# Kernel tuning notes

Hardware: AMD Instinct MI355X
Metric: run time of the kernel (lower is better)

The kernel has to match this reference:

```python
import jax, jax.numpy as jnp
import numpy as np

DIM = 1024
HEADS = 16
DIM_HEAD = 64
NB_FEATURES = 266
EPS = 1e-4


def _gaussian_orthogonal_random_matrix(nb_rows, nb_cols, seed=0):
    # Blocks of orthogonal rows (QR of gaussian), rows rescaled by gaussian row norms (scaling=0).
    rng = np.random.default_rng(seed)
    blocks = []
    full, rem = divmod(nb_rows, nb_cols)
    for _ in range(full):
        g = rng.standard_normal((nb_cols, nb_cols))
        q, _ = np.linalg.qr(g)
        blocks.append(q.T)
    if rem > 0:
        g = rng.standard_normal((nb_cols, nb_cols))
        q, _ = np.linalg.qr(g)
        blocks.append(q.T[:rem])
    mat = np.concatenate(blocks, axis=0)
    multiplier = np.linalg.norm(rng.standard_normal((nb_rows, nb_cols)), axis=1)
    return (multiplier[:, None] * mat).astype(np.float32)


def _softmax_kernel(data, proj, is_query):
    # data: [b,h,n,d], proj: [m,d]
    d = data.shape[-1]
    data_normalizer = d ** -0.25
    ratio = proj.shape[0] ** -0.5
    data_dash = jnp.einsum('bhnd,md->bhnm', data * data_normalizer, proj)
    diag = 0.5 * (data_normalizer ** 2) * jnp.sum(data * data, axis=-1, keepdims=True)
    if is_query:
        m = jax.lax.stop_gradient(jnp.max(data_dash, axis=-1, keepdims=True))
    else:
        m = jax.lax.stop_gradient(jnp.max(data_dash, axis=(-1, -2), keepdims=True))
    return ratio * (jnp.exp(data_dash - diag - m) + EPS)


def _linear_attention(q, k, v):
    # q,k: [b,h,n,m], v: [b,h,n,e]
    k_cumsum = jnp.sum(k, axis=-2)                                   # [b,h,m]
    D_inv = 1.0 / jnp.einsum('bhnm,bhm->bhn', q, k_cumsum)           # [b,h,n]
    context = jnp.einsum('bhnm,bhne->bhme', k, v)                    # [b,h,m,e]
    return jnp.einsum('bhme,bhnm,bhn->bhne', context, q, D_inv)      # [b,h,n,e]


def setup_inputs() -> dict:
    key = jax.random.key(0)
    k1, k2, k3, k4, k5 = jax.random.split(key, 5)
    B, N = 2, 4096
    inner = HEADS * DIM_HEAD
    s = DIM ** -0.5
    return {
        'x': jax.random.normal(k1, (B, N, DIM), dtype=jnp.float32),
        'Wq': jax.random.normal(k2, (inner, DIM), dtype=jnp.float32) * s,
        'Wk': jax.random.normal(k3, (inner, DIM), dtype=jnp.float32) * s,
        'Wv': jax.random.normal(k4, (inner, DIM), dtype=jnp.float32) * s,
        'Wo': jax.random.normal(k5, (DIM, inner), dtype=jnp.float32) * s,
        'bo': jnp.zeros((DIM,), dtype=jnp.float32),
        'proj': jnp.asarray(_gaussian_orthogonal_random_matrix(NB_FEATURES, DIM_HEAD)),
    }


def reference(x, Wq, Wk, Wv, Wo, bo, proj):
    b, n, _ = x.shape
    def split_heads(t):
        return t.reshape(b, n, HEADS, DIM_HEAD).transpose(0, 2, 1, 3)  # [b,h,n,d]
    q = split_heads(x @ Wq.T)
    k = split_heads(x @ Wk.T)
    v = split_heads(x @ Wv.T)
    qp = _softmax_kernel(q, proj, is_query=True)
    kp = _softmax_kernel(k, proj, is_query=False)
    out = _linear_attention(qp, kp, v)                                # [b,h,n,d]
    out = out.transpose(0, 2, 1, 3).reshape(b, n, HEADS * DIM_HEAD)
    return out @ Wo.T + bo
```

## Files before the change

### kernel.cpp

```cpp
#include <hip/hip_runtime.h>
#include <hip/hip_bf16.h>
#include <hip/hip_fp16.h>


#define B_   2
#define N_   4096
#define H_   16
#define M_   266
#define MP_  288
#define DIM_ 1024
#define RT_  8192
#define BH_  32
#define LKN  40
#define LSB  296
#define NCH  16
#define KS_  8

typedef __attribute__((ext_vector_type(8))) short s8v;
typedef __attribute__((ext_vector_type(4))) float f4v;

__device__ __forceinline__ ushort f2bu(float x){ __hip_bfloat16 h = __float2bfloat16(x); return *(ushort*)&h; }
__device__ __forceinline__ float  bu2f(ushort u){ return __uint_as_float(((unsigned)u) << 16); }

constexpr float NORMC  = 0.35355339059327379f;
constexpr float RATIOC = 0.06131393f;
constexpr float DIAGC  = 0.0625f;
constexpr float EPSC   = 1e-4f;

__device__ __forceinline__ void stf(float* p, float v){ *p = v; }
__device__ __forceinline__ void stf(__hip_bfloat16* p, float v){ *p = __float2bfloat16(v); }

__device__ __forceinline__ void gl_lds16(const ushort* g, ushort* l){
    __builtin_amdgcn_global_load_lds(
        (const __attribute__((address_space(1))) unsigned int*)(const unsigned int*)g,
        (__attribute__((address_space(3))) unsigned int*)(unsigned int*)l,
        16, 0, 0);
}

__device__ __forceinline__ void cast8(const float* __restrict__ s, ushort* __restrict__ d, int i){
    const float4 a = *(const float4*)&s[i];
    const float4 b = *(const float4*)&s[i + 4];
    ushort4 lo, hi;
    lo.x = f2bu(a.x); lo.y = f2bu(a.y); lo.z = f2bu(a.z); lo.w = f2bu(a.w);
    hi.x = f2bu(b.x); hi.y = f2bu(b.y); hi.z = f2bu(b.z); hi.w = f2bu(b.w);
    *(ushort4*)&d[i]     = lo;
    *(ushort4*)&d[i + 4] = hi;
}

__global__ void cast_all(const float* __restrict__ x,
                         const float* __restrict__ Wq, const float* __restrict__ Wk,
                         const float* __restrict__ Wv, const float* __restrict__ Wo,
                         const float* __restrict__ proj,
                         ushort* __restrict__ xb,
                         ushort* __restrict__ Wqb, ushort* __restrict__ Wkb,
                         ushort* __restrict__ Wvb, ushort* __restrict__ Wob,
                         ushort* __restrict__ projb)
{
    const int bid = blockIdx.x, tid = threadIdx.x;
    if (bid < 4096) {
        cast8(x, xb, (bid * 256 + tid) * 8);
    } else if (bid < 6144) {
        const int w = (bid - 4096) >> 9;
        const float* s; ushort* d;
        switch (w) {
            case 0:  s = Wq; d = Wqb; break;
            case 1:  s = Wk; d = Wkb; break;
            case 2:  s = Wv; d = Wvb; break;
            default: s = Wo; d = Wob; break;
        }
        cast8(s, d, (((bid - 4096) & 511) * 256 + tid) * 8);
    } else {
        const int i = (bid - 6144) * 256 + tid;
        const int m = i >> 6, dc = i & 63;
        projb[i] = f2bu((m < M_) ? NORMC * proj[m * 64 + dc] : 0.f);
    }
}

template<bool DIAG, bool BIAS, typename TC>
__launch_bounds__(256)
__global__ void gemm128(const ushort* __restrict__ A, const ushort* __restrict__ Bw,
                        const float* __restrict__ bias, TC* __restrict__ C,
                        float* __restrict__ diag)
{
    __shared__ ushort As[128 * 32];
    __shared__ ushort Bs[128 * 32];

    const int tid  = threadIdx.x;
    const int lane = tid & 63, wave = tid >> 6;
    const int col  = lane & 15, quad = lane >> 4;
    const int wm   = (wave & 1) * 64, wn = (wave >> 1) * 64;

    const int gX = gridDim.x, total = gX * gridDim.y, cpx = total >> 3;
    const int fl = blockIdx.x + blockIdx.y * gX;
    const int sw = (fl & 7) * cpx + (fl >> 3);
    const int r0 = (sw / gX) * 128, c0 = (sw % gX) * 128;

    const int f0 = tid * 8;
    const int row0 = f0 >> 5, kc0 = f0 & 31;
    const size_t aoff0 = (size_t)(r0 + row0) * DIM_ + kc0;
    const size_t aoff1 = (size_t)(r0 + 64 + row0) * DIM_ + kc0;
    const size_t boff0 = (size_t)(c0 + row0) * DIM_ + kc0;
    const size_t boff1 = (size_t)(c0 + 64 + row0) * DIM_ + kc0;
    ushort* asb0 = &As[wave * 512];
    ushort* asb1 = &As[2048 + wave * 512];
    ushort* bsb0 = &Bs[wave * 512];
    ushort* bsb1 = &Bs[2048 + wave * 512];

    f4v acc[4][4];
    #pragma unroll
    for (int i = 0; i < 4; ++i)
        #pragma unroll
        for (int j = 0; j < 4; ++j) acc[i][j] = (f4v){0.f, 0.f, 0.f, 0.f};

    for (int kk = 0; kk < DIM_; kk += 32) {
        gl_lds16(&A[aoff0 + kk],  asb0);
        gl_lds16(&A[aoff1 + kk],  asb1);
        gl_lds16(&Bw[boff0 + kk], bsb0);
        gl_lds16(&Bw[boff1 + kk], bsb1);
        __syncthreads();
        s8v af[4], bf[4];
        #pragma unroll
        for (int i = 0; i < 4; ++i)
            af[i] = *(const s8v*)&As[(wm + i * 16 + col) * 32 + quad * 8];
        #pragma unroll
        for (int j = 0; j < 4; ++j)
            bf[j] = *(const s8v*)&Bs[(wn + j * 16 + col) * 32 + quad * 8];
        #pragma unroll
        for (int i = 0; i < 4; ++i)
            #pragma unroll
            for (int j = 0; j < 4; ++j)
                acc[i][j] = __builtin_amdgcn_mfma_f32_16x16x32_bf16(af[i], bf[j], acc[i][j], 0, 0, 0);
        __syncthreads();
    }

    float bb[4] = {0.f, 0.f, 0.f, 0.f};
    if (BIAS) {
        #pragma unroll
        for (int j = 0; j < 4; ++j) bb[j] = bias[c0 + wn + j * 16 + col];
    }
    #pragma unroll
    for (int i = 0; i < 4; ++i) {
        #pragma unroll
        for (int r = 0; r < 4; ++r) {
            const size_t grow = (size_t)(r0 + wm + i * 16 + quad * 4 + r);
            #pragma unroll
            for (int j = 0; j < 4; ++j)
                stf(&C[grow * DIM_ + c0 + wn + j * 16 + col], acc[i][j][r] + bb[j]);
        }
    }
    if (DIAG) {
        const int hglob = (c0 + wn) >> 6;
        #pragma unroll
        for (int i = 0; i < 4; ++i) {
            #pragma unroll
            for (int r = 0; r < 4; ++r) {
                float s = 0.f;
                #pragma unroll
                for (int j = 0; j < 4; ++j) s += acc[i][j][r] * acc[i][j][r];
                s += __shfl_xor(s, 1); s += __shfl_xor(s, 2);
                s += __shfl_xor(s, 4); s += __shfl_xor(s, 8);
                if (col == 0)
                    diag[(size_t)(r0 + wm + i * 16 + quad * 4 + r) * H_ + hglob] = DIAGC * s;
            }
        }
    }
}

__launch_bounds__(256)
__global__ void gemm128_qkv(const ushort* __restrict__ A, const ushort* __restrict__ Bw,
                            ushort* __restrict__ Q, ushort* __restrict__ K,
                            ushort* __restrict__ V,
                            float* __restrict__ diagQ, float* __restrict__ diagK)
{
    __shared__ ushort As[128 * 32];
    __shared__ ushort Bs[128 * 32];

    const int tid  = threadIdx.x;
    const int lane = tid & 63, wave = tid >> 6;
    const int col  = lane & 15, quad = lane >> 4;
    const int wm   = (wave & 1) * 64, wn = (wave >> 1) * 64;

    const int fl = blockIdx.x + blockIdx.y * 24;
    const int sw = (fl & 7) * 192 + (fl >> 3);
    const int r0 = (sw / 24) * 128, c0 = (sw % 24) * 128;

    const int f0 = tid * 8;
    const int row0 = f0 >> 5, kc0 = f0 & 31;
    const size_t aoff0 = (size_t)(r0 + row0) * DIM_ + kc0;
    const size_t aoff1 = (size_t)(r0 + 64 + row0) * DIM_ + kc0;
    const size_t boff0 = (size_t)(c0 + row0) * DIM_ + kc0;
    const size_t boff1 = (size_t)(c0 + 64 + row0) * DIM_ + kc0;
    ushort* asb0 = &As[wave * 512];
    ushort* asb1 = &As[2048 + wave * 512];
    ushort* bsb0 = &Bs[wave * 512];
    ushort* bsb1 = &Bs[2048 + wave * 512];

    f4v acc[4][4];
    #pragma unroll
    for (int i = 0; i < 4; ++i)
        #pragma unroll
        for (int j = 0; j < 4; ++j) acc[i][j] = (f4v){0.f, 0.f, 0.f, 0.f};

    for (int kk = 0; kk < DIM_; kk += 32) {
        gl_lds16(&A[aoff0 + kk],  asb0);
        gl_lds16(&A[aoff1 + kk],  asb1);
        gl_lds16(&Bw[boff0 + kk], bsb0);
        gl_lds16(&Bw[boff1 + kk], bsb1);
        __syncthreads();
        s8v af[4], bf[4];
        #pragma unroll
        for (int i = 0; i < 4; ++i)
            af[i] = *(const s8v*)&As[(wm + i * 16 + col) * 32 + quad * 8];
        #pragma unroll
        for (int j = 0; j < 4; ++j)
            bf[j] = *(const s8v*)&Bs[(wn + j * 16 + col) * 32 + quad * 8];
        #pragma unroll
        for (int i = 0; i < 4; ++i)
            #pragma unroll
            for (int j = 0; j < 4; ++j)
                acc[i][j] = __builtin_amdgcn_mfma_f32_16x16x32_bf16(af[i], bf[j], acc[i][j], 0, 0, 0);
        __syncthreads();
    }

    const int which = c0 >> 10;
    const int cc    = c0 & 1023;
    ushort* C = (which == 0) ? Q : ((which == 1) ? K : V);
    float* dptr = (which == 0) ? diagQ : ((which == 1) ? diagK : nullptr);

    #pragma unroll
    for (int i = 0; i < 4; ++i) {
        #pragma unroll
        for (int r = 0; r < 4; ++r) {
            const size_t grow = (size_t)(r0 + wm + i * 16 + quad * 4 + r);
            #pragma unroll
            for (int j = 0; j < 4; ++j)
                C[grow * DIM_ + cc + wn + j * 16 + col] = f2bu(acc[i][j][r]);
        }
    }
    if (dptr) {
        const int hglob = (cc + wn) >> 6;
        #pragma unroll
        for (int i = 0; i < 4; ++i) {
            #pragma unroll
            for (int r = 0; r < 4; ++r) {
                float s = 0.f;
                #pragma unroll
                for (int j = 0; j < 4; ++j) s += acc[i][j][r] * acc[i][j][r];
                s += __shfl_xor(s, 1); s += __shfl_xor(s, 2);
                s += __shfl_xor(s, 4); s += __shfl_xor(s, 8);
                if (col == 0)
                    dptr[(size_t)(r0 + wm + i * 16 + quad * 4 + r) * H_ + hglob] = DIAGC * s;
            }
        }
    }
}

__launch_bounds__(256)
__global__ void kctx_mfma(const ushort* __restrict__ Kb, const ushort* __restrict__ Vb,
                          const ushort* __restrict__ projb,
                          const float* __restrict__ diagK,
                          float* __restrict__ ctxp, float* __restrict__ kcsp,
                          float* __restrict__ vsump, float* __restrict__ kmaxp)
{
    __shared__ ushort Pl[MP_ * 64];
    __shared__ ushort Kp[MP_ * LKN];
    __shared__ ushort Vt[64 * LKN];
    __shared__ float kred[2][MP_];
    __shared__ float wmx[4];

    const int tid  = threadIdx.x;
    const int lane = tid & 63, wave = tid >> 6;
    const int col  = lane & 15, quad = lane >> 4;
    const int bh   = blockIdx.y, b = bh >> 4, h = bh & 15;
    const int n0   = blockIdx.x * (N_ / NCH);
    const int rowblk = wave >> 1;
    const int t0 = (wave & 1) * 9;

    for (int i = tid; i < MP_ * 8; i += 256) {
        const int m = i >> 3, c = i & 7;
        *(uint4*)&Pl[m * 64 + ((c ^ (m & 7)) << 3)] = *(const uint4*)&projb[m * 64 + (c << 3)];
    }
    const int sw0 = (quad ^ (col & 7)) << 3;
    const int sw1 = ((quad | 4) ^ (col & 7)) << 3;
    __syncthreads();

    float mx = -3.4e38f;
    {
        size_t arA = ((size_t)(b * N_ + n0 + rowblk * 16 + col)) * DIM_ + h * 64 + quad * 8;
        s8v pA0 = *(const s8v*)&Kb[arA];
        s8v pA1 = *(const s8v*)&Kb[arA + 32];
        for (int ks = 0; ks < KS_; ++ks) {
            const s8v a0 = pA0, a1 = pA1;
            if (ks + 1 < KS_) {
                arA += (size_t)32 * DIM_;
                pA0 = *(const s8v*)&Kb[arA];
                pA1 = *(const s8v*)&Kb[arA + 32];
            }
            for (int t = t0; t < t0 + 9; ++t) {
                const s8v bf0 = *(const s8v*)&Pl[(t * 16 + col) * 64 + sw0];
                const s8v bf1 = *(const s8v*)&Pl[(t * 16 + col) * 64 + sw1];
                f4v a = (f4v){0.f, 0.f, 0.f, 0.f};
                a = __builtin_amdgcn_mfma_f32_16x16x32_bf16(a0, bf0, a, 0, 0, 0);
                a = __builtin_amdgcn_mfma_f32_16x16x32_bf16(a1, bf1, a, 0, 0, 0);
                if (t * 16 + col < M_) {
                    #pragma unroll
                    for (int r = 0; r < 4; ++r) mx = fmaxf(mx, a[r]);
                }
            }
        }
    }
    #pragma unroll
    for (int o = 32; o > 0; o >>= 1) mx = fmaxf(mx, __shfl_xor(mx, o));
    if (lane == 0) wmx[wave] = mx;
    __syncthreads();
    const float mc = fmaxf(fmaxf(wmx[0], wmx[1]), fmaxf(wmx[2], wmx[3]));
    if (tid == 0) kmaxp[bh * NCH + blockIdx.x] = mc;

    const int nst = tid & 31, est = (tid >> 5) * 8;
    s8v vvP = *(const s8v*)&Vb[((size_t)(b * N_ + n0 + nst)) * DIM_ + h * 64 + est];
    const size_t arow0 = ((size_t)(b * N_ + n0 + rowblk * 16 + col)) * DIM_ + h * 64 + quad * 8;
    s8v afP0 = *(const s8v*)&Kb[arow0];
    s8v afP1 = *(const s8v*)&Kb[arow0 + 32];
    float dgrP[4];
    #pragma unroll
    for (int r = 0; r < 4; ++r)
        dgrP[r] = diagK[((size_t)(b * N_ + n0 + rowblk * 16 + quad * 4 + r)) * H_ + h];

    f4v facc[18];
    #pragma unroll
    for (int t = 0; t < 18; ++t) facc[t] = (f4v){0.f, 0.f, 0.f, 0.f};
    float kcsa[9] = {};
    float vsa[8] = {};

    for (int ks = 0; ks < KS_; ++ks) {
        const s8v vv = vvP, af0 = afP0, af1 = afP1;
        float dgr[4];
        #pragma unroll
        for (int r = 0; r < 4; ++r) dgr[r] = dgrP[r];

        #pragma unroll
        for (int j = 0; j < 8; ++j) {
            const ushort uv = ((const ushort*)&vv)[j];
            Vt[(est + j) * LKN + nst] = uv;
            vsa[j] += bu2f(uv);
        }

        for (int t = t0; t < t0 + 9; ++t) {
            const s8v bf0 = *(const s8v*)&Pl[(t * 16 + col) * 64 + sw0];
            const s8v bf1 = *(const s8v*)&Pl[(t * 16 + col) * 64 + sw1];
            f4v a = (f4v){0.f, 0.f, 0.f, 0.f};
            a = __builtin_amdgcn_mfma_f32_16x16x32_bf16(af0, bf0, a, 0, 0, 0);
            a = __builtin_amdgcn_mfma_f32_16x16x32_bf16(af1, bf1, a, 0, 0, 0);
            const int m = t * 16 + col;
            float kp[4];
            #pragma unroll
            for (int r = 0; r < 4; ++r) {
                float v = 0.f;
                if (m < M_) v = __expf(a[r] - dgr[r] - mc);
                kp[r] = v;
            }
            kcsa[t - t0] += kp[0] + kp[1] + kp[2] + kp[3];
            ushort4 pk;
            pk.x = f2bu(kp[0]); pk.y = f2bu(kp[1]); pk.z = f2bu(kp[2]); pk.w = f2bu(kp[3]);
            *(ushort4*)&Kp[m * LKN + rowblk * 16 + quad * 4] = pk;
        }

        if (ks + 1 < KS_) {
            const int nb1 = n0 + (ks + 1) * 32;
            vvP  = *(const s8v*)&Vb[((size_t)(b * N_ + nb1 + nst)) * DIM_ + h * 64 + est];
            const size_t arow1 = ((size_t)(b * N_ + nb1 + rowblk * 16 + col)) * DIM_ + h * 64 + quad * 8;
            afP0 = *(const s8v*)&Kb[arow1];
            afP1 = *(const s8v*)&Kb[arow1 + 32];
            #pragma unroll
            for (int r = 0; r < 4; ++r)
                dgrP[r] = diagK[((size_t)(b * N_ + nb1 + rowblk * 16 + quad * 4 + r)) * H_ + h];
        }
        __syncthreads();
        const s8v bfe = *(const s8v*)&Vt[(wave * 16 + col) * LKN + quad * 8];
        #pragma unroll
        for (int t = 0; t < 18; ++t) {
            const s8v am = *(const s8v*)&Kp[(t * 16 + col) * LKN + quad * 8];
            facc[t] = __builtin_amdgcn_mfma_f32_16x16x32_bf16(am, bfe, facc[t], 0, 0, 0);
        }
        __syncthreads();
    }

    const size_t pbase = ((size_t)bh * NCH + blockIdx.x) * (MP_ * 64);
    #pragma unroll
    for (int t = 0; t < 18; ++t) {
        #pragma unroll
        for (int r = 0; r < 4; ++r)
            __builtin_nontemporal_store(facc[t][r],
                &ctxp[pbase + (size_t)(t * 16 + quad * 4 + r) * 64 + wave * 16 + col]);
    }
    #pragma unroll
    for (int j = 0; j < 8; ++j) {
        float s = vsa[j];
        s += __shfl_xor(s, 1);  s += __shfl_xor(s, 2);
        s += __shfl_xor(s, 4);  s += __shfl_xor(s, 8);
        s += __shfl_xor(s, 16);
        if ((lane & 31) == 0)
            vsump[((size_t)bh * NCH + blockIdx.x) * 64 + est + j] = s;
    }
    for (int t = t0; t < t0 + 9; ++t) {
        float s = kcsa[t - t0];
        s += __shfl_xor(s, 16);
        s += __shfl_xor(s, 32);
        if (quad == 0) kred[rowblk][t * 16 + col] = s;
    }
    __syncthreads();
    for (int i = tid; i < MP_; i += 256)
        kcsp[((size_t)bh * NCH + blockIdx.x) * MP_ + i] = kred[0][i] + kred[1][i];
}

__launch_bounds__(256)
__global__ void ctx_reduce(const float* __restrict__ ctxp, const float* __restrict__ kcsp,
                           const float* __restrict__ vsump, const float* __restrict__ kmaxp,
                           ushort* __restrict__ ctxT, float* __restrict__ kcs)
{
    __shared__ float scl[NCH];
    __shared__ float vsl[64];
    const int bh = blockIdx.y, tid = threadIdx.x;

    if (tid < NCH) {
        float M = -3.4e38f;
        #pragma unroll
        for (int c = 0; c < NCH; ++c) M = fmaxf(M, kmaxp[bh * NCH + c]);
        scl[tid] = __expf(kmaxp[bh * NCH + tid] - M);
    }
    if (tid >= 64 && tid < 128) {
        const int e = tid - 64;
        float s = 0.f;
        #pragma unroll
        for (int c = 0; c < NCH; ++c) s += vsump[((size_t)bh * NCH + c) * 64 + e];
        vsl[e] = s;
    }
    __syncthreads();

    const int base = blockIdx.x * (MP_ * 64 / 8);
    const size_t cb = (size_t)bh * NCH * (MP_ * 64);
    #pragma unroll
    for (int u = 0; u < 9; ++u) {
        const int flat = base + u * 256 + tid;
        float s = 0.f;
        #pragma unroll
        for (int c = 0; c < NCH; ++c)
            s += scl[c] * __builtin_nontemporal_load(&ctxp[cb + (size_t)c * (MP_ * 64) + flat]);
        const int m = flat >> 6, e = flat & 63;
        ctxT[((size_t)bh * 64 + e) * MP_ + m] = f2bu(RATIOC * (s + EPSC * vsl[e]));
    }
    if (blockIdx.x == 0) {
        for (int i = tid; i < MP_; i += 256) {
            float s = 0.f;
            #pragma unroll
            for (int c = 0; c < NCH; ++c) s += scl[c] * kcsp[((size_t)bh * NCH + c) * MP_ + i];
            kcs[(size_t)bh * MP_ + i] = RATIOC * (s + EPSC * (float)N_);
        }
    }
}

__launch_bounds__(256)
__global__ void qdashout(const ushort* __restrict__ Qb, const ushort* __restrict__ projb,
                         const float* __restrict__ diagQ, const float* __restrict__ kcs,
                         const ushort* __restrict__ ctxT, ushort* __restrict__ Ab)
{
    __shared__ ushort SB[64 * LSB];
    __shared__ float kcl[MP_];
    __shared__ float dinv[64];

    const int tid  = threadIdx.x;
    const int lane = tid & 63, wave = tid >> 6;
    const int col  = lane & 15, quad = lane >> 4;
    const int bh   = blockIdx.y, b = bh >> 4, h = bh & 15;
    const int n0   = blockIdx.x * 64;

    const size_t arow = ((size_t)(b * N_ + n0 + wave * 16 + col)) * DIM_ + h * 64 + quad * 8;
    const s8v af0 = *(const s8v*)&Qb[arow];
    const s8v af1 = *(const s8v*)&Qb[arow + 32];
    float dgr[4];
    #pragma unroll
    for (int r = 0; r < 4; ++r)
        dgr[r] = diagQ[((size_t)(b * N_ + n0 + wave * 16 + quad * 4 + r)) * H_ + h];

    for (int i = tid; i < MP_ * 8; i += 256) {
        const int m = i >> 3, c = i & 7;
        *(uint4*)&SB[m * 64 + ((c ^ (m & 7)) << 3)] = *(const uint4*)&projb[m * 64 + (c << 3)];
    }
    for (int i = tid; i < MP_; i += 256) kcl[i] = kcs[(size_t)bh * MP_ + i];
    __syncthreads();

    const int sw0 = (quad ^ (col & 7)) << 3;
    const int sw1 = ((quad | 4) ^ (col & 7)) << 3;

    f4v acc[17];
    #pragma unroll
    for (int t = 0; t < 17; ++t) {
        const s8v bf0 = *(const s8v*)&SB[(t * 16 + col) * 64 + sw0];
        const s8v bf1 = *(const s8v*)&SB[(t * 16 + col) * 64 + sw1];
        f4v a = (f4v){0.f, 0.f, 0.f, 0.f};
        a = __builtin_amdgcn_mfma_f32_16x16x32_bf16(af0, bf0, a, 0, 0, 0);
        a = __builtin_amdgcn_mfma_f32_16x16x32_bf16(af1, bf1, a, 0, 0, 0);
        acc[t] = a;
    }

    float rmx[4];
    #pragma unroll
    for (int r = 0; r < 4; ++r) {
        float mx = -3.4e38f;
        #pragma unroll
        for (int t = 0; t < 16; ++t) mx = fmaxf(mx, acc[t][r]);
        if (col < 10) mx = fmaxf(mx, acc[16][r]);
        mx = fmaxf(mx, __shfl_xor(mx, 1));
        mx = fmaxf(mx, __shfl_xor(mx, 2));
        mx = fmaxf(mx, __shfl_xor(mx, 4));
        mx = fmaxf(mx, __shfl_xor(mx, 8));
        rmx[r] = mx;
    }

    float den[4] = {0.f, 0.f, 0.f, 0.f};
    #pragma unroll
    for (int t = 0; t < 17; ++t) {
        const int m = t * 16 + col;
        const float kc = kcl[m];
        #pragma unroll
        for (int r = 0; r < 4; ++r) {
            float v = 0.f;
            if (m < M_)
                v = RATIOC * (__expf(acc[t][r] - dgr[r] - rmx[r]) + EPSC);
            acc[t][r] = v;
            den[r] += v * kc;
        }
    }

    const ushort* ct = ctxT + (size_t)bh * 64 * MP_;
    s8v bfA[4], bfB[4];
    #pragma unroll
    for (int j = 0; j < 4; ++j)
        bfA[j] = *(const s8v*)&ct[(size_t)(j * 16 + col) * MP_ + quad * 8];

    __syncthreads();

    #pragma unroll
    for (int r = 0; r < 4; ++r) {
        const int rb = (wave * 16 + quad * 4 + r) * LSB;
        #pragma unroll
        for (int t = 0; t < 17; ++t)
            SB[rb + t * 16 + col] = f2bu(acc[t][r]);
        if (col < 8) *(uint*)&SB[rb + 272 + col * 2] = 0u;
    }
    #pragma unroll
    for (int r = 0; r < 4; ++r) {
        float d = den[r];
        d += __shfl_xor(d, 1); d += __shfl_xor(d, 2);
        d += __shfl_xor(d, 4); d += __shfl_xor(d, 8);
        if (col == 0)
            dinv[wave * 16 + quad * 4 + r] = 1.0f / fmaxf(d, 1e-30f);
    }
    __syncthreads();

    f4v acc2[4];
    #pragma unroll
    for (int j = 0; j < 4; ++j) acc2[j] = (f4v){0.f, 0.f, 0.f, 0.f};
    #pragma unroll
    for (int kp = 0; kp < 4; ++kp) {
        const int k0 = 2 * kp, k1 = 2 * kp + 1, k2 = 2 * kp + 2;
        #pragma unroll
        for (int j = 0; j < 4; ++j)
            bfB[j] = *(const s8v*)&ct[(size_t)(j * 16 + col) * MP_ + k1 * 32 + quad * 8];
        const s8v afrA = *(const s8v*)&SB[(wave * 16 + col) * LSB + k0 * 32 + quad * 8];
        #pragma unroll
        for (int j = 0; j < 4; ++j)
            acc2[j] = __builtin_amdgcn_mfma_f32_16x16x32_bf16(afrA, bfA[j], acc2[j], 0, 0, 0);
        #pragma unroll
        for (int j = 0; j < 4; ++j)
            bfA[j] = *(const s8v*)&ct[(size_t)(j * 16 + col) * MP_ + k2 * 32 + quad * 8];
        const s8v afrB = *(const s8v*)&SB[(wave * 16 + col) * LSB + k1 * 32 + quad * 8];
        #pragma unroll
        for (int j = 0; j < 4; ++j)
            acc2[j] = __builtin_amdgcn_mfma_f32_16x16x32_bf16(afrB, bfB[j], acc2[j], 0, 0, 0);
    }
    {
        const s8v afrT = *(const s8v*)&SB[(wave * 16 + col) * LSB + 8 * 32 + quad * 8];
        #pragma unroll
        for (int j = 0; j < 4; ++j)
            acc2[j] = __builtin_amdgcn_mfma_f32_16x16x32_bf16(afrT, bfA[j], acc2[j], 0, 0, 0);
    }
    #pragma unroll
    for (int j = 0; j < 4; ++j) {
        #pragma unroll
        for (int r = 0; r < 4; ++r) {
            const int n = wave * 16 + quad * 4 + r;
            Ab[((size_t)(b * N_ + n0 + n)) * DIM_ + h * 64 + j * 16 + col] =
                f2bu(acc2[j][r] * dinv[n]);
        }
    }
}

extern "C" void kernel_launch(void* const* d_in, const int* in_sizes, int n_in,
                              void* d_out, int out_size, void* d_ws, size_t ws_size,
                              hipStream_t stream)
{
    const float* x    = (const float*)d_in[0];
    const float* Wq   = (const float*)d_in[1];
    const float* Wk   = (const float*)d_in[2];
    const float* Wv   = (const float*)d_in[3];
    const float* Wo   = (const float*)d_in[4];
    const float* bo   = (const float*)d_in[5];
    const float* proj = (const float*)d_in[6];

    char* ws = (char*)d_ws;
    size_t o = 0;
    ushort* xb    = (ushort*)(ws + o); o += (size_t)RT_ * DIM_ * 2;
    ushort* Wqb   = (ushort*)(ws + o); o += (size_t)DIM_ * DIM_ * 2;
    ushort* Wkb   = (ushort*)(ws + o); o += (size_t)DIM_ * DIM_ * 2;
    ushort* Wvb   = (ushort*)(ws + o); o += (size_t)DIM_ * DIM_ * 2;
    ushort* Wob   = (ushort*)(ws + o); o += (size_t)DIM_ * DIM_ * 2;
    ushort* projb = (ushort*)(ws + o); o += (size_t)MP_ * 64 * 2;
    ushort* Qb    = (ushort*)(ws + o); o += (size_t)RT_ * DIM_ * 2;
    ushort* Kb    = (ushort*)(ws + o); o += (size_t)RT_ * DIM_ * 2;
    ushort* Vb    = (ushort*)(ws + o); o += (size_t)RT_ * DIM_ * 2;
    ushort* Ab    = (ushort*)(ws + o); o += (size_t)RT_ * DIM_ * 2;
    float*    ctxp  = (float*)(ws + o);    o += (size_t)BH_ * NCH * MP_ * 64 * 4;
    float*    kcsp  = (float*)(ws + o);    o += (size_t)BH_ * NCH * MP_ * 4;
    float*    kcs   = (float*)(ws + o);    o += (size_t)BH_ * MP_ * 4;
    float*    vsump = (float*)(ws + o);    o += (size_t)BH_ * NCH * 64 * 4;
    float*    kmaxp = (float*)(ws + o);    o += (size_t)BH_ * NCH * 4;
    float*    diagQ = (float*)(ws + o);    o += (size_t)RT_ * H_ * 4;
    float*    diagK = (float*)(ws + o);    o += (size_t)RT_ * H_ * 4;
    ushort*   ctxT  = (ushort*)(ws + o);   o += (size_t)BH_ * 64 * MP_ * 2;

    cast_all<<<dim3(6216), 256, 0, stream>>>(x, Wq, Wk, Wv, Wo, proj,
                                             xb, Wqb, Wkb, Wvb, Wob, projb);

    gemm128_qkv<<<dim3(24, RT_ / 128), 256, 0, stream>>>(xb, Wqb, Qb, Kb, Vb, diagQ, diagK);

    kctx_mfma<<<dim3(NCH, BH_), 256, 0, stream>>>(Kb, Vb, projb, diagK, ctxp, kcsp, vsump, kmaxp);
    ctx_reduce<<<dim3(8, BH_), 256, 0, stream>>>(ctxp, kcsp, vsump, kmaxp, ctxT, kcs);
    qdashout<<<dim3(N_ / 64, BH_), 256, 0, stream>>>(Qb, projb, diagQ, kcs, ctxT, Ab);

    gemm128<false, true, float><<<dim3(DIM_ / 128, RT_ / 128), 256, 0, stream>>>(Ab, Wob, bo, (float*)d_out, nullptr);
}
```

Baseline: 280.8 us.

## Use online running max for key features instead of a separate max pass

Removes the first pass over the key chunk that recomputed the K·proj MFMAs only to find the block maximum. Each step now computes the projections once, takes a per-step block max, and rescales the accumulated context and key sums whenever the running max grows, as in online softmax. This halves the projection MFMAs and K reloads. In exchange it adds an extra barrier per step, keeps nine accumulator tiles live in registers (more register pressure), and may rescale the accumulators.

After: 286.9 us. +2.2%, slower.

```diff
diff --git a/kernel.cpp b/kernel.cpp
--- a/kernel.cpp
+++ b/kernel.cpp
@@ -282,39 +282,6 @@
     }
     const int sw0 = (quad ^ (col & 7)) << 3;
     const int sw1 = ((quad | 4) ^ (col & 7)) << 3;
-    __syncthreads();
-
-    float mx = -3.4e38f;
-    {
-        size_t arA = ((size_t)(b * N_ + n0 + rowblk * 16 + col)) * DIM_ + h * 64 + quad * 8;
-        s8v pA0 = *(const s8v*)&Kb[arA];
-        s8v pA1 = *(const s8v*)&Kb[arA + 32];
-        for (int ks = 0; ks < KS_; ++ks) {
-            const s8v a0 = pA0, a1 = pA1;
-            if (ks + 1 < KS_) {
-                arA += (size_t)32 * DIM_;
-                pA0 = *(const s8v*)&Kb[arA];
-                pA1 = *(const s8v*)&Kb[arA + 32];
-            }
-            for (int t = t0; t < t0 + 9; ++t) {
-                const s8v bf0 = *(const s8v*)&Pl[(t * 16 + col) * 64 + sw0];
-                const s8v bf1 = *(const s8v*)&Pl[(t * 16 + col) * 64 + sw1];
-                f4v a = (f4v){0.f, 0.f, 0.f, 0.f};
-                a = __builtin_amdgcn_mfma_f32_16x16x32_bf16(a0, bf0, a, 0, 0, 0);
-                a = __builtin_amdgcn_mfma_f32_16x16x32_bf16(a1, bf1, a, 0, 0, 0);
-                if (t * 16 + col < M_) {
-                    #pragma unroll
-                    for (int r = 0; r < 4; ++r) mx = fmaxf(mx, a[r]);
-                }
-            }
-        }
-    }
-    #pragma unroll
-    for (int o = 32; o > 0; o >>= 1) mx = fmaxf(mx, __shfl_xor(mx, o));
-    if (lane == 0) wmx[wave] = mx;
-    __syncthreads();
-    const float mc = fmaxf(fmaxf(wmx[0], wmx[1]), fmaxf(wmx[2], wmx[3]));
-    if (tid == 0) kmaxp[bh * NCH + blockIdx.x] = mc;
 
     const int nst = tid & 31, est = (tid >> 5) * 8;
     s8v vvP = *(const s8v*)&Vb[((size_t)(b * N_ + n0 + nst)) * DIM_ + h * 64 + est];
@@ -331,6 +298,9 @@
     for (int t = 0; t < 18; ++t) facc[t] = (f4v){0.f, 0.f, 0.f, 0.f};
     float kcsa[9] = {};
     float vsa[8] = {};
+    float m_run = -3.4e38f;
+
+    __syncthreads();
 
     for (int ks = 0; ks < KS_; ++ks) {
         const s8v vv = vvP, af0 = afP0, af1 = afP1;
@@ -345,25 +315,29 @@
             vsa[j] += bu2f(uv);
         }
 
-        for (int t = t0; t < t0 + 9; ++t) {
+        f4v dd[9];
+        #pragma unroll
+        for (int tt = 0; tt < 9; ++tt) {
+            const int t = t0 + tt;
             const s8v bf0 = *(const s8v*)&Pl[(t * 16 + col) * 64 + sw0];
             const s8v bf1 = *(const s8v*)&Pl[(t * 16 + col) * 64 + sw1];
             f4v a = (f4v){0.f, 0.f, 0.f, 0.f};
             a = __builtin_amdgcn_mfma_f32_16x16x32_bf16(af0, bf0, a, 0, 0, 0);
             a = __builtin_amdgcn_mfma_f32_16x16x32_bf16(af1, bf1, a, 0, 0, 0);
-            const int m = t * 16 + col;
-            float kp[4];
-            #pragma unroll
-            for (int r = 0; r < 4; ++r) {
-                float v = 0.f;
-                if (m < M_) v = __expf(a[r] - dgr[r] - mc);
-                kp[r] = v;
+            dd[tt] = a;
+        }
+
+        float mx = -3.4e38f;
+        #pragma unroll
+        for (int tt = 0; tt < 9; ++tt) {
+            if ((t0 + tt) * 16 + col < M_) {
+                #pragma unroll
+                for (int r = 0; r < 4; ++r) mx = fmaxf(mx, dd[tt][r]);
             }
-            kcsa[t - t0] += kp[0] + kp[1] + kp[2] + kp[3];
-            ushort4 pk;
-            pk.x = f2bu(kp[0]); pk.y = f2bu(kp[1]); pk.z = f2bu(kp[2]); pk.w = f2bu(kp[3]);
-            *(ushort4*)&Kp[m * LKN + rowblk * 16 + quad * 4] = pk;
-        }
+        }
+        #pragma unroll
+        for (int o = 32; o > 0; o >>= 1) mx = fmaxf(mx, __shfl_xor(mx, o));
+        if (lane == 0) wmx[wave] = mx;
 
         if (ks + 1 < KS_) {
             const int nb1 = n0 + (ks + 1) * 32;
@@ -376,6 +350,37 @@
                 dgrP[r] = diagK[((size_t)(b * N_ + nb1 + rowblk * 16 + quad * 4 + r)) * H_ + h];
         }
         __syncthreads();
+
+        const float bmax = fmaxf(fmaxf(wmx[0], wmx[1]), fmaxf(wmx[2], wmx[3]));
+        if (bmax > m_run) {
+            const float s = __expf(m_run - bmax);
+            m_run = bmax;
+            #pragma unroll
+            for (int t = 0; t < 18; ++t) {
+                #pragma unroll
+                for (int r = 0; r < 4; ++r) facc[t][r] *= s;
+            }
+            #pragma unroll
+            for (int u = 0; u < 9; ++u) kcsa[u] *= s;
+        }
+
+        #pragma unroll
+        for (int tt = 0; tt < 9; ++tt) {
+            const int m = (t0 + tt) * 16 + col;
+            float kp[4];
+            #pragma unroll
+            for (int r = 0; r < 4; ++r) {
+                float v = 0.f;
+                if (m < M_) v = __expf(dd[tt][r] - dgr[r] - m_run);
+                kp[r] = v;
+            }
+            kcsa[tt] += kp[0] + kp[1] + kp[2] + kp[3];
+            ushort4 pk;
+            pk.x = f2bu(kp[0]); pk.y = f2bu(kp[1]); pk.z = f2bu(kp[2]); pk.w = f2bu(kp[3]);
+            *(ushort4*)&Kp[m * LKN + rowblk * 16 + quad * 4] = pk;
+        }
+        __syncthreads();
+
         const s8v bfe = *(const s8v*)&Vt[(wave * 16 + col) * LKN + quad * 8];
         #pragma unroll
         for (int t = 0; t < 18; ++t) {
@@ -384,6 +389,8 @@
         }
         __syncthreads();
     }
+
+    if (tid == 0) kmaxp[bh * NCH + blockIdx.x] = m_run;
 
     const size_t pbase = ((size_t)bh * NCH + blockIdx.x) * (MP_ * 64);
     #pragma unroll
@@ -402,11 +409,11 @@
         if ((lane & 31) == 0)
             vsump[((size_t)bh * NCH + blockIdx.x) * 64 + est + j] = s;
     }
-    for (int t = t0; t < t0 + 9; ++t) {
-        float s = kcsa[t - t0];
+    for (int tt = 0; tt < 9; ++tt) {
+        float s = kcsa[tt];
         s += __shfl_xor(s, 16);
         s += __shfl_xor(s, 32);
-        if (quad == 0) kred[rowblk][t * 16 + col] = s;
+        if (quad == 0) kred[rowblk][(t0 + tt) * 16 + col] = s;
     }
     __syncthreads();
     for (int i = tid; i < MP_; i += 256)
```
